# Kernel tuning notes

Measured on AMD Instinct MI355X. Metric: run time of the kernel, lower is better.

Reference implementation:

```python
import jax, jax.numpy as jnp
import numpy as np

C, H, K, G = 256, 8, 32, 8
HD = C // H
SCALE = HD ** -0.5
POS_BND = int(0.8 * K * 1 ** 0.5)  # 25
RPE_NUM = 2 * POS_BND + 1          # 51
NW = 4096


def setup_inputs() -> dict:
    key = jax.random.key(0)
    ks = jax.random.split(key, 8)
    data = jax.random.normal(ks[0], (NW * (K + G), C), dtype=jnp.float32)
    # relative xyz offsets between points in a window; exercise the clamp
    rel_pos = jax.random.randint(ks[1], (NW, K, K, 3), -POS_BND - 5, POS_BND + 6).astype(jnp.int32)
    # additive mask: 0 for valid pairs, -100 for masked (padded) pairs
    keep = jax.random.bernoulli(ks[2], 0.9, (NW, K + G, K + G))
    mask = jnp.where(keep, 0.0, -100.0).astype(jnp.float32)
    qkv_w = jax.random.normal(ks[3], (C, 3 * C), dtype=jnp.float32) * (C ** -0.5)
    qkv_b = jnp.zeros((3 * C,), dtype=jnp.float32)
    proj_w = jax.random.normal(ks[4], (C, C), dtype=jnp.float32) * (C ** -0.5)
    proj_b = jnp.zeros((C,), dtype=jnp.float32)
    rpe_table = jax.random.normal(ks[5], (3 * RPE_NUM, H), dtype=jnp.float32) * 0.02
    return {"data": data, "rel_pos": rel_pos, "mask": mask, "qkv_w": qkv_w,
            "qkv_b": qkv_b, "proj_w": proj_w, "proj_b": proj_b, "rpe_table": rpe_table}


def reference(data, rel_pos, mask, qkv_w, qkv_b, proj_w, proj_b, rpe_table):
    W = K + G  # window size including context tokens
    qkv = data @ qkv_w + qkv_b                              # (T, 3C)
    qkv_std = jnp.std(qkv, axis=0, ddof=1)                  # torch .std is unbiased
    qkv = qkv.reshape(-1, W, 3, H, HD).transpose(2, 0, 3, 1, 4)  # (3, Nw, H, W, HD)
    q, k, v = qkv[0] * SCALE, qkv[1], qkv[2]
    attn = jnp.einsum('nhqd,nhkd->nhqk', q, k)              # (Nw, H, W, W)
    # RPE: clamp offsets, index per-axis slices of table, sum over xyz
    idx = jnp.clip(rel_pos, -POS_BND, POS_BND) + POS_BND + jnp.arange(3, dtype=rel_pos.dtype) * RPE_NUM
    rpe = rpe_table[idx].sum(axis=3)                        # (Nw, K, K, H)
    rpe = rpe.transpose(0, 3, 1, 2)                         # (Nw, H, K, K)
    rpe = jnp.pad(rpe, ((0, 0), (0, 0), (G, 0), (G, 0)))    # pad for context tokens
    attn = attn + rpe + mask[:, None]
    attn = jax.nn.softmax(attn, axis=-1)
    out = jnp.einsum('nhqk,nhkd->nqhd', attn, v).reshape(-1, W, C)
    out = out @ proj_w + proj_b                             # (Nw, W, C)
    return (out, qkv_std)
```

## Files before the change

kernel.cpp:

```cpp
#include <hip/hip_runtime.h>
#include <math.h>

#define SCALE_F 0.17677669529663687f

typedef __bf16 bf16x8 __attribute__((ext_vector_type(8)));
typedef float f32x4 __attribute__((ext_vector_type(4)));

__device__ __forceinline__ unsigned short f2bf(float f) {
  unsigned u = __builtin_bit_cast(unsigned, f);
  u = (u + 0x7FFFu + ((u >> 16) & 1u)) >> 16;
  return (unsigned short)u;
}
__device__ __forceinline__ float bf2f(unsigned short u) {
  return __builtin_bit_cast(float, (unsigned)u << 16);
}
__device__ __forceinline__ unsigned pk2(float a, float b) {
  return (unsigned)f2bf(a) | ((unsigned)f2bf(b) << 16);
}
__device__ __forceinline__ bf16x8 ld16(const void* p) {
  int4 v = *(const int4*)p;
  return __builtin_bit_cast(bf16x8, v);
}
__device__ __forceinline__ void gll16(const void* g, void* l) {
  __builtin_amdgcn_global_load_lds(
      (const __attribute__((address_space(1))) unsigned int*)g,
      (__attribute__((address_space(3))) unsigned int*)l, 16, 0, 0);
}


__global__ void octa_prep2(const float* __restrict__ qkv_w, const float* __restrict__ proj_w,
                           unsigned short* __restrict__ wTq, unsigned short* __restrict__ pTq)
{
  int e = blockIdx.x * 256 + threadIdx.x;
  if (e < 196608) {
    int c = e >> 13;
    int nc = c >> 3, kc = c & 7;
    int p2 = e & 8191;
    int n = p2 >> 5, cw = p2 & 31;
    int kl = cw ^ (((n >> 1) & 3) << 3);
    wTq[e] = f2bf(qkv_w[(size_t)(kc * 32 + kl) * 768 + nc * 256 + n]);
  } else {
    int e2 = e - 196608;
    int kc = e2 >> 13, p2 = e2 & 8191;
    int n = p2 >> 5, cw = p2 & 31;
    int kl = cw ^ (((n >> 1) & 3) << 3);
    pTq[e2] = f2bf(proj_w[(size_t)(kc * 32 + kl) * 256 + n]);
  }
}

#define KQ_A0 0
#define KQ_A1 8192
#define KQ_B0 16384
#define KQ_B1 32768
#define KQ_LDS 49152

__global__ __launch_bounds__(512, 4)
void octa_qkv(const float* __restrict__ data, const float* __restrict__ qkv_b,
              const unsigned short* __restrict__ wTq, float* __restrict__ ws,
              char* __restrict__ qg, char* __restrict__ kg, char* __restrict__ vg)
{
  extern __shared__ char smem[];
  const int tid = threadIdx.x, lane = tid & 63, wid = tid >> 6;
  const int ql = lane & 15, lg = lane >> 4;
  const int bm = blockIdx.x / 3, nc = blockIdx.x - bm * 3;
  const int wr = wid >> 2, wc = wid & 3;
  const char* wbase = (const char*)wTq + (size_t)nc * 131072;

  const int arow = tid >> 2, aq = tid & 3;
  const float* abase = data + ((size_t)bm * 128 + arow) * 256 + aq * 8;
  const int alds = arow * 64 + ((aq * 16) ^ (((arow >> 1) & 3) << 4));

  float4 a0 = *(const float4*)abase;
  float4 a1 = *(const float4*)(abase + 4);
  gll16(wbase + wid * 1024 + lane * 16, smem + KQ_B0 + wid * 1024);
  gll16(wbase + 8192 + wid * 1024 + lane * 16, smem + KQ_B0 + 8192 + wid * 1024);
  *(uint2*)(smem + KQ_A0 + alds) = make_uint2(pk2(a0.x, a0.y), pk2(a0.z, a0.w));
  *(uint2*)(smem + KQ_A0 + alds + 8) = make_uint2(pk2(a1.x, a1.y), pk2(a1.z, a1.w));
  __syncthreads();

  f32x4 acc[4][4];
  #pragma unroll
  for (int m = 0; m < 4; ++m)
    #pragma unroll
    for (int n = 0; n < 4; ++n) acc[m][n] = (f32x4){0.f, 0.f, 0.f, 0.f};

  #pragma unroll
  for (int t = 0; t < 8; ++t) {
    float4 na0, na1;
    if (t < 7) {
      na0 = *(const float4*)(abase + (t + 1) * 32);
      na1 = *(const float4*)(abase + (t + 1) * 32 + 4);
      const char* bsrc = wbase + (size_t)(t + 1) * 16384;
      char* bb1 = smem + (((t + 1) & 1) ? KQ_B1 : KQ_B0);
      gll16(bsrc + wid * 1024 + lane * 16, bb1 + wid * 1024);
      gll16(bsrc + 8192 + wid * 1024 + lane * 16, bb1 + 8192 + wid * 1024);
    }
    const char* ab = smem + ((t & 1) ? KQ_A1 : KQ_A0);
    const char* bb = smem + ((t & 1) ? KQ_B1 : KQ_B0);
    bf16x8 af[4], bf[4];
    #pragma unroll
    for (int mt = 0; mt < 4; ++mt) {
      int row = wr * 64 + mt * 16 + ql;
      af[mt] = ld16(ab + row * 64 + ((lg * 16) ^ (((row >> 1) & 3) << 4)));
    }
    #pragma unroll
    for (int nt = 0; nt < 4; ++nt) {
      int n = wc * 64 + nt * 16 + ql;
      bf[nt] = ld16(bb + n * 64 + ((lg * 16) ^ (((n >> 1) & 3) << 4)));
    }
    #pragma unroll
    for (int nt = 0; nt < 4; ++nt)
      #pragma unroll
      for (int mt = 0; mt < 4; ++mt)
        acc[mt][nt] = __builtin_amdgcn_mfma_f32_16x16x32_bf16(af[mt], bf[nt], acc[mt][nt], 0, 0, 0);
    if (t < 7) {
      char* ab1 = smem + (((t + 1) & 1) ? KQ_A1 : KQ_A0);
      *(uint2*)(ab1 + alds) = make_uint2(pk2(na0.x, na0.y), pk2(na0.z, na0.w));
      *(uint2*)(ab1 + alds + 8) = make_uint2(pk2(na1.x, na1.y), pk2(na1.z, na1.w));
    }
    __syncthreads();
  }

  char* base = nc == 0 ? qg : (nc == 1 ? kg : vg);
  const float cs = (nc == 0) ? SCALE_F : 1.0f;
  #pragma unroll
  for (int nt = 0; nt < 4; ++nt) {
    int col = wc * 64 + nt * 16 + ql;
    int h = col >> 5, d = col & 31;
    float bias = qkv_b[nc * 256 + col];
    float s1 = 0.f, s2 = 0.f;
    #pragma unroll
    for (int mt = 0; mt < 4; ++mt) {
      int tg0 = bm * 128 + wr * 64 + mt * 16 + lg * 4;
      int w = tg0 / 40, tk0 = tg0 - w * 40;
      size_t slice = (size_t)(w * 8 + h) * 2560;
      #pragma unroll
      for (int r = 0; r < 4; ++r) {
        float v = acc[mt][nt][r] + bias;
        s1 += v; s2 += v * v;
        *(unsigned short*)(base + slice + (tk0 + r) * 64 + d * 2) = f2bf(v * cs);
      }
    }
    s1 += __shfl_xor(s1, 16); s1 += __shfl_xor(s1, 32);
    s2 += __shfl_xor(s2, 16); s2 += __shfl_xor(s2, 32);
    if (lg == 0) {
      atomicAdd(ws + nc * 256 + col, s1);
      atomicAdd(ws + 768 + nc * 256 + col, s2);
    }
  }
}

#define A2_MSK 0
#define A2_IDX 4160
#define A2_RPT 8256
#define A2_P   13376
#define A2_LDS 44096

__global__ __launch_bounds__(512, 4)
void octa_attn(const char* __restrict__ qg, const char* __restrict__ kg,
               const char* __restrict__ vg, const float* __restrict__ maskp,
               const int* __restrict__ rel_pos, const float* __restrict__ rpe_table,
               char* __restrict__ Og)
{
  extern __shared__ char smem[];
  const int tid = threadIdx.x, w = blockIdx.x, wid = tid >> 6;
  const int lane = tid & 63, ql = lane & 15, lg = lane >> 4, h = wid;
  const int perm = ql * 64 + lg * 16;
  const char* qb = qg + (size_t)(w * 8 + h) * 2560;
  const char* kb = kg + (size_t)(w * 8 + h) * 2560;
  const char* vb = vg + (size_t)(w * 8 + h) * 2560;

  bf16x8 kf0 = ld16(kb + perm), kf1 = ld16(kb + 1024 + perm), kf2 = ld16(kb + 2048 + perm);
  bf16x8 qf0 = ld16(qb + perm), qf1 = ld16(qb + 1024 + perm), qf2 = ld16(qb + 2048 + perm);
  union U8 { unsigned short u[8]; bf16x8 v; };
  U8 ua, ub, uc, ud;
  #pragma unroll
  for (int j = 0; j < 8; ++j) {
    int tok = lg * 8 + j;
    ua.u[j] = *(const unsigned short*)(vb + tok * 64 + ql * 2);
    ub.u[j] = *(const unsigned short*)(vb + tok * 64 + (16 + ql) * 2);
  }
  if (lg == 0) {
    #pragma unroll
    for (int j = 0; j < 8; ++j) {
      uc.u[j] = *(const unsigned short*)(vb + (32 + j) * 64 + ql * 2);
      ud.u[j] = *(const unsigned short*)(vb + (32 + j) * 64 + (16 + ql) * 2);
    }
  } else {
    #pragma unroll
    for (int j = 0; j < 8; ++j) { uc.u[j] = 0; ud.u[j] = 0; }
  }
  bf16x8 vA = ua.v, vB = ub.v, vC = uc.v, vD = ud.v;

  for (int f = tid; f < 1600; f += 512) {
    float m = maskp[(size_t)w * 1600 + f];
    int qi = f / 40, kj = f - qi * 40;
    *(unsigned short*)(smem + A2_MSK + kj * 104 + qi * 2) = f2bf(m);
  }
  for (int f = tid; f < 1024; f += 512) {
    const int* rp = rel_pos + ((size_t)w * 1024 + f) * 3;
    int c0 = rp[0], c1 = rp[1], c2 = rp[2];
    c0 = min(25, max(-25, c0)); c1 = min(25, max(-25, c1)); c2 = min(25, max(-25, c2));
    unsigned pk = (unsigned)(c0 + 25) | ((unsigned)(c1 + 76) << 10) | ((unsigned)(c2 + 127) << 20);
    int qi8 = f >> 5, kj8 = f & 31;
    *(unsigned*)(smem + A2_IDX + kj8 * 128 + ((qi8 * 4) ^ ((kj8 & 1) << 6))) = pk;
  }
  for (int f = tid; f < 1224; f += 512)
    *(float*)(smem + A2_RPT + (((f & 7) * 160 + (f >> 3)) << 2)) = rpe_table[f];
  __syncthreads();

  f32x4 st[9];
  {
    bf16x8 kf[3] = {kf0, kf1, kf2}, qf[3] = {qf0, qf1, qf2};
    #pragma unroll
    for (int a = 0; a < 3; ++a)
      #pragma unroll
      for (int b = 0; b < 3; ++b)
        st[a * 3 + b] = __builtin_amdgcn_mfma_f32_16x16x32_bf16(
            kf[a], qf[b], (f32x4){0.f, 0.f, 0.f, 0.f}, 0, 0, 0);
  }

  float mx[3] = {-3e38f, -3e38f, -3e38f};
  #pragma unroll
  for (int a = 0; a < 3; ++a) {
    #pragma unroll
    for (int b = 0; b < 3; ++b) {
      #pragma unroll
      for (int r = 0; r < 4; ++r) {
        int kj = a * 16 + lg * 4 + r;
        int qi = b * 16 + ql;
        float s = st[a * 3 + b][r];
        if (kj < 40) {
          if (qi < 40) {
            s += bf2f(*(const unsigned short*)(smem + A2_MSK + kj * 104 + qi * 2));
            if (kj >= 8 && qi >= 8) {
              unsigned pk = *(const unsigned*)(smem + A2_IDX + (kj - 8) * 128 +
                                               (((qi - 8) * 4) ^ (((kj - 8) & 1) << 6)));
              s += *(const float*)(smem + A2_RPT + ((h * 160 + (pk & 1023)) << 2))
                 + *(const float*)(smem + A2_RPT + ((h * 160 + ((pk >> 10) & 1023)) << 2))
                 + *(const float*)(smem + A2_RPT + ((h * 160 + (pk >> 20)) << 2));
            }
          }
        } else {
          s = -1e30f;
        }
        st[a * 3 + b][r] = s;
        mx[b] = fmaxf(mx[b], s);
      }
    }
  }
  #pragma unroll
  for (int b = 0; b < 3; ++b) {
    mx[b] = fmaxf(mx[b], __shfl_xor(mx[b], 16));
    mx[b] = fmaxf(mx[b], __shfl_xor(mx[b], 32));
  }
  float sum[3] = {0.f, 0.f, 0.f};
  #pragma unroll
  for (int a = 0; a < 3; ++a)
    #pragma unroll
    for (int b = 0; b < 3; ++b)
      #pragma unroll
      for (int r = 0; r < 4; ++r) {
        float e = __expf(st[a * 3 + b][r] - mx[b]);
        st[a * 3 + b][r] = e;
        sum[b] += e;
      }
  float inv[3];
  #pragma unroll
  for (int b = 0; b < 3; ++b) {
    sum[b] += __shfl_xor(sum[b], 16);
    sum[b] += __shfl_xor(sum[b], 32);
    inv[b] = 1.f / sum[b];
  }

  char* pb_ = smem + A2_P + wid * 3840;
  f32x4 ot[6];
  #pragma unroll
  for (int i = 0; i < 6; ++i) ot[i] = (f32x4){0.f, 0.f, 0.f, 0.f};

  #pragma unroll
  for (int a = 0; a < 2; ++a)
    #pragma unroll
    for (int b = 0; b < 3; ++b)
      #pragma unroll
      for (int r = 0; r < 4; ++r) {
        int kj = a * 16 + lg * 4 + r, qi = b * 16 + ql;
        *(unsigned short*)(pb_ + qi * 80 + kj * 2) = f2bf(st[a * 3 + b][r] * inv[b]);
      }
  asm volatile("" ::: "memory");
  #pragma unroll
  for (int b = 0; b < 3; ++b) {
    bf16x8 pf = ld16(pb_ + (b * 16 + ql) * 80 + lg * 16);
    ot[b]     = __builtin_amdgcn_mfma_f32_16x16x32_bf16(vA, pf, ot[b], 0, 0, 0);
    ot[3 + b] = __builtin_amdgcn_mfma_f32_16x16x32_bf16(vB, pf, ot[3 + b], 0, 0, 0);
  }
  asm volatile("" ::: "memory");
  #pragma unroll
  for (int b = 0; b < 3; ++b) {
    int qi = b * 16 + ql;
    #pragma unroll
    for (int r = 0; r < 4; ++r)
      *(unsigned short*)(pb_ + qi * 80 + (lg * 4 + r) * 2) = f2bf(st[6 + b][r] * inv[b]);
    *(uint2*)(pb_ + qi * 80 + 32 + lg * 8) = make_uint2(0u, 0u);
  }
  asm volatile("" ::: "memory");
  #pragma unroll
  for (int b = 0; b < 3; ++b) {
    bf16x8 pf = ld16(pb_ + (b * 16 + ql) * 80 + lg * 16);
    ot[b]     = __builtin_amdgcn_mfma_f32_16x16x32_bf16(vC, pf, ot[b], 0, 0, 0);
    ot[3 + b] = __builtin_amdgcn_mfma_f32_16x16x32_bf16(vD, pf, ot[3 + b], 0, 0, 0);
  }

  __syncthreads();
  #pragma unroll
  for (int dm = 0; dm < 2; ++dm)
    #pragma unroll
    for (int b = 0; b < 3; ++b) {
      int qi = b * 16 + ql;
      if (b == 2 && ql >= 8) continue;
      unsigned u0 = pk2(ot[dm * 3 + b][0], ot[dm * 3 + b][1]);
      unsigned u1 = pk2(ot[dm * 3 + b][2], ot[dm * 3 + b][3]);
      int tg = w * 40 + qi;
      int colb = (h * 32 + dm * 16 + lg * 4) * 2;
      *(uint2*)(Og + (size_t)tg * 512 + (colb ^ (((tg >> 1) & 3) << 4))) = make_uint2(u0, u1);
    }
}

#define P3_A0 0
#define P3_A1 8192
#define P3_B0 16384
#define P3_B1 32768
#define P3_LDS 49152

__global__ __launch_bounds__(512, 4)
void octa_proj(const char* __restrict__ Og, const unsigned short* __restrict__ pTq,
               const float* __restrict__ proj_b, float* __restrict__ out)
{
  extern __shared__ char smem[];
  const int tid = threadIdx.x, lane = tid & 63, wid = tid >> 6;
  const int ql = lane & 15, lg = lane >> 4;
  const int bm = blockIdx.x;
  const int wr = wid >> 2, wc = wid & 3;
  const char* pbase = (const char*)pTq;

  gll16(Og + ((size_t)bm * 128 + (tid >> 2)) * 512 + (tid & 3) * 16,
        smem + P3_A0 + wid * 1024);
  #pragma unroll
  for (int it = 0; it < 2; ++it)
    gll16(pbase + (wid * 128 + it * 64 + lane) * 16, smem + P3_B0 + wid * 2048 + it * 1024);
  __syncthreads();

  f32x4 acc[4][4];
  #pragma unroll
  for (int m = 0; m < 4; ++m)
    #pragma unroll
    for (int n = 0; n < 4; ++n) acc[m][n] = (f32x4){0.f, 0.f, 0.f, 0.f};

  #pragma unroll
  for (int t = 0; t < 8; ++t) {
    if (t < 7) {
      char* ab1 = smem + (((t + 1) & 1) ? P3_A1 : P3_A0);
      char* bb1 = smem + (((t + 1) & 1) ? P3_B1 : P3_B0);
      gll16(Og + ((size_t)bm * 128 + (tid >> 2)) * 512 + (t + 1) * 64 + (tid & 3) * 16,
            ab1 + wid * 1024);
      #pragma unroll
      for (int it = 0; it < 2; ++it)
        gll16(pbase + (size_t)(t + 1) * 16384 + (wid * 128 + it * 64 + lane) * 16,
              bb1 + wid * 2048 + it * 1024);
    }
    const char* ab = smem + ((t & 1) ? P3_A1 : P3_A0);
    const char* bb = smem + ((t & 1) ? P3_B1 : P3_B0);
    bf16x8 af[4];
    #pragma unroll
    for (int mt = 0; mt < 4; ++mt) {
      int row = wr * 64 + mt * 16 + ql;
      af[mt] = ld16(ab + row * 64 + ((lg * 16) ^ (((row >> 1) & 3) << 4)));
    }
    #pragma unroll
    for (int nt = 0; nt < 4; ++nt) {
      int n = wc * 64 + nt * 16 + ql;
      bf16x8 bf = ld16(bb + n * 64 + ((lg * 16) ^ (((n >> 1) & 3) << 4)));
      #pragma unroll
      for (int mt = 0; mt < 4; ++mt)
        acc[mt][nt] = __builtin_amdgcn_mfma_f32_16x16x32_bf16(af[mt], bf, acc[mt][nt], 0, 0, 0);
    }
    __syncthreads();
  }

  #pragma unroll
  for (int nt = 0; nt < 4; ++nt) {
    int col = wc * 64 + nt * 16 + ql;
    float pb = proj_b[col];
    #pragma unroll
    for (int mt = 0; mt < 4; ++mt)
      #pragma unroll
      for (int r = 0; r < 4; ++r) {
        int tg = bm * 128 + wr * 64 + mt * 16 + lg * 4 + r;
        out[(size_t)tg * 256 + col] = acc[mt][nt][r] + pb;
      }
  }
}

__global__ void octa_std(const float* __restrict__ ws, float* __restrict__ out,
                         int total_rows, size_t off)
{
  int j = blockIdx.x * 256 + threadIdx.x;
  if (j < 768) {
    float s = ws[j], ss = ws[768 + j];
    float T = (float)total_rows;
    float var = (ss - s * s / T) / (T - 1.f);
    out[off + j] = sqrtf(fmaxf(var, 0.f));
  }
}

#define O_RPE 0
#define O_MSK 4896
#define O_IDX 8096
#define O_A   12192
#define O_ATT 36768
#define B1_SZ 49152
#define ATT_STRIDE 11776
#define AK 3840
#define AV 7680
#define B2_S (O_ATT + 94208)
#define B2_A O_ATT
#define LDS_BYTES_V4 163744

__device__ __forceinline__ int a_addr(int row, int byte) {
  return O_A + row * 512 + (byte ^ ((row & 7) << 4));
}
__device__ __forceinline__ int v_addr(int d, int byte) {
  return AV + d * 128 + (byte ^ ((d & 7) << 4));
}

__global__ void octa_prep_v4(const float* __restrict__ qkv_w, const float* __restrict__ proj_w,
                             unsigned short* __restrict__ wTq, unsigned short* __restrict__ pTq)
{
  int idx = blockIdx.x * 256 + threadIdx.x;
  if (idx < 196608) {
    int n = idx >> 8, k = idx & 255;
    wTq[idx] = f2bf(qkv_w[k * 768 + n]);
  } else {
    int i = idx - 196608;
    int n = i >> 8, k = i & 255;
    pTq[i] = f2bf(proj_w[k * 256 + n]);
  }
}

__global__ __launch_bounds__(512, 2)
void octa_main_v4(const float* __restrict__ data, const int* __restrict__ rel_pos,
                  const float* __restrict__ maskp, const float* __restrict__ qkv_b,
                  const float* __restrict__ proj_b, const float* __restrict__ rpe_table,
                  const unsigned short* __restrict__ wTq, const unsigned short* __restrict__ pTq,
                  float* __restrict__ ws, float* __restrict__ out)
{
  extern __shared__ char smem[];
  float* s_rpe = (float*)(smem + O_RPE);
  const int tid = threadIdx.x;
  const int w   = blockIdx.x;
  const int wid = tid >> 6;
  const int lane = tid & 63;
  const int ql = lane & 15;
  const int lg = lane >> 4;
  const int h  = wid;
  const int ab = O_ATT + wid * ATT_STRIDE;

  {
    #pragma unroll
    for (int it = 0; it < 6; ++it) {
      int g = it * 512 + tid;
      int n = g >> 2, slot = g & 3;
      const char* src = (const char*)wTq + (size_t)n * 512 + ((slot * 16) ^ ((n & 3) << 4));
      gll16(src, smem + O_ATT + it * 8192 + wid * 1024);
    }
  }
  for (int f = tid; f < 1224; f += 512) s_rpe[f] = rpe_table[f];
  for (int f = tid; f < 400; f += 512) {
    float4 m4 = ((const float4*)(maskp + (size_t)w * 1600))[f];
    uint2 pk;
    pk.x = pk2(m4.x, m4.y); pk.y = pk2(m4.z, m4.w);
    *(uint2*)(smem + O_MSK + f * 8) = pk;
  }
  for (int p = tid; p < 1024; p += 512) {
    const int* rp = rel_pos + ((size_t)w * 1024 + p) * 3;
    int c0 = rp[0], c1 = rp[1], c2 = rp[2];
    c0 = min(25, max(-25, c0)); c1 = min(25, max(-25, c1)); c2 = min(25, max(-25, c2));
    unsigned pk = (unsigned)(c0 + 25) | ((unsigned)(c1 + 76) << 10) | ((unsigned)(c2 + 127) << 20);
    *(unsigned*)(smem + O_IDX + ((p * 4) ^ (((p >> 5) & 7) << 4))) = pk;
  }
  {
    const float4* src = (const float4*)(data + (size_t)w * 10240);
    for (int f = tid; f < 2560; f += 512) {
      int token = f >> 6, q4 = f & 63;
      float4 d4 = src[f];
      uint2 pk;
      pk.x = pk2(d4.x, d4.y); pk.y = pk2(d4.z, d4.w);
      *(uint2*)(smem + a_addr(token, q4 * 8)) = pk;
    }
    int token = 40 + (tid >> 6), byte = (tid & 63) * 8;
    *(uint2*)(smem + a_addr(token, byte)) = make_uint2(0u, 0u);
  }
  __syncthreads();

  f32x4 acc[18];
  #pragma unroll
  for (int i = 0; i < 18; ++i) acc[i] = (f32x4){0.f, 0.f, 0.f, 0.f};

  for (int t = 0; t < 8; ++t) {
    if (t < 7) {
      int bb = O_ATT + ((t + 1) & 1) * B1_SZ;
      #pragma unroll
      for (int it = 0; it < 6; ++it) {
        int g = it * 512 + tid;
        int n = g >> 2, slot = g & 3;
        const char* src = (const char*)wTq + (size_t)n * 512 + (t + 1) * 64
                          + ((slot * 16) ^ ((n & 3) << 4));
        gll16(src, smem + bb + it * 8192 + wid * 1024);
      }
    }
    const int bb = O_ATT + (t & 1) * B1_SZ;
    bf16x8 af[3];
    #pragma unroll
    for (int mt = 0; mt < 3; ++mt)
      af[mt] = ld16(smem + a_addr(mt * 16 + ql, t * 64 + lg * 16));
    #pragma unroll
    for (int j = 0; j < 6; ++j) {
      int n = ((j >> 1) * 16 + 2 * wid + (j & 1)) * 16 + ql;
      bf16x8 bf = ld16(smem + bb + n * 64 + ((lg * 16) ^ ((n & 3) << 4)));
      #pragma unroll
      for (int mt = 0; mt < 3; ++mt)
        acc[j * 3 + mt] = __builtin_amdgcn_mfma_f32_16x16x32_bf16(af[mt], bf, acc[j * 3 + mt], 0, 0, 0);
    }
    __syncthreads();
  }

  {
    #pragma unroll
    for (int it = 0; it < 4; ++it) {
      int g = it * 512 + tid;
      int n = g >> 3, slot = g & 7;
      const char* src = (const char*)pTq + (size_t)n * 512 + ((slot * 16) ^ ((n & 7) << 4));
      gll16(src, smem + B2_S + it * 8192 + wid * 1024);
    }
  }

  #pragma unroll
  for (int j = 0; j < 6; ++j) {
    int sec = j >> 1;
    int ncol = sec * 256 + 32 * wid + (j & 1) * 16 + ql;
    int d = (j & 1) * 16 + ql;
    float bias = qkv_b[ncol];
// ... 66 lines not shown
        mx[b] = fmaxf(mx[b], s);
      }
    }
  }
  #pragma unroll
  for (int b = 0; b < 3; ++b) {
    mx[b] = fmaxf(mx[b], __shfl_xor(mx[b], 16));
    mx[b] = fmaxf(mx[b], __shfl_xor(mx[b], 32));
  }
  float sum[3] = {0.f, 0.f, 0.f};
  #pragma unroll
  for (int a = 0; a < 3; ++a)
    #pragma unroll
    for (int b = 0; b < 3; ++b)
      #pragma unroll
      for (int r = 0; r < 4; ++r) {
        float e = __expf(st[a * 3 + b][r] - mx[b]);
        st[a * 3 + b][r] = e;
        sum[b] += e;
      }
  float inv[3];
  #pragma unroll
  for (int b = 0; b < 3; ++b) {
    sum[b] += __shfl_xor(sum[b], 16);
    sum[b] += __shfl_xor(sum[b], 32);
    inv[b] = 1.f / sum[b];
  }

  f32x4 ot[6];
  #pragma unroll
  for (int i = 0; i < 6; ++i) ot[i] = (f32x4){0.f, 0.f, 0.f, 0.f};

  #pragma unroll
  for (int a = 0; a < 2; ++a)
    #pragma unroll
    for (int b = 0; b < 3; ++b)
      #pragma unroll
      for (int r = 0; r < 4; ++r) {
        int kj = a * 16 + lg * 4 + r, qi = b * 16 + ql;
        *(unsigned short*)(smem + ab + qi * 80 + kj * 2) = f2bf(st[a * 3 + b][r] * inv[b]);
      }
  asm volatile("" ::: "memory");
  {
    bf16x8 vf0 = ld16(smem + ab + v_addr(ql, lg * 16));
    bf16x8 vf1 = ld16(smem + ab + v_addr(16 + ql, lg * 16));
    #pragma unroll
    for (int b = 0; b < 3; ++b) {
      bf16x8 pf = ld16(smem + ab + (b * 16 + ql) * 80 + lg * 16);
      ot[b] = __builtin_amdgcn_mfma_f32_16x16x32_bf16(vf0, pf, ot[b], 0, 0, 0);
      ot[3 + b] = __builtin_amdgcn_mfma_f32_16x16x32_bf16(vf1, pf, ot[3 + b], 0, 0, 0);
    }
  }
  asm volatile("" ::: "memory");
  #pragma unroll
  for (int b = 0; b < 3; ++b) {
    int qi = b * 16 + ql;
    #pragma unroll
    for (int r = 0; r < 4; ++r) {
      int kj = 32 + lg * 4 + r;
      *(unsigned short*)(smem + ab + qi * 80 + (kj - 32) * 2) = f2bf(st[6 + b][r] * inv[b]);
    }
    *(uint2*)(smem + ab + qi * 80 + 32 + lg * 8) = make_uint2(0u, 0u);
  }
  asm volatile("" ::: "memory");
  {
    bf16x8 vf0 = ld16(smem + ab + v_addr(ql, 64 + lg * 16));
    bf16x8 vf1 = ld16(smem + ab + v_addr(16 + ql, 64 + lg * 16));
    #pragma unroll
    for (int b = 0; b < 3; ++b) {
      bf16x8 pf = ld16(smem + ab + (b * 16 + ql) * 80 + lg * 16);
      ot[b] = __builtin_amdgcn_mfma_f32_16x16x32_bf16(vf0, pf, ot[b], 0, 0, 0);
      ot[3 + b] = __builtin_amdgcn_mfma_f32_16x16x32_bf16(vf1, pf, ot[3 + b], 0, 0, 0);
    }
  }
  #pragma unroll
  for (int dm = 0; dm < 2; ++dm)
    #pragma unroll
    for (int b = 0; b < 3; ++b)
      #pragma unroll
      for (int r = 0; r < 4; ++r) {
        int d = dm * 16 + lg * 4 + r;
        int qi = b * 16 + ql;
        *(unsigned short*)(smem + a_addr(qi, (h * 32 + d) * 2)) = f2bf(ot[dm * 3 + b][r]);
      }
  __syncthreads();

  f32x4 oacc[6];
  #pragma unroll
  for (int i = 0; i < 6; ++i) oacc[i] = (f32x4){0.f, 0.f, 0.f, 0.f};

  for (int t = 0; t < 4; ++t) {
    if (t < 3) {
      int bb = ((t + 1) & 1) ? B2_A : B2_S;
      #pragma unroll
      for (int it = 0; it < 4; ++it) {
        int g = it * 512 + tid;
        int n = g >> 3, slot = g & 7;
        const char* src = (const char*)pTq + (size_t)n * 512 + (t + 1) * 128
                          + ((slot * 16) ^ ((n & 7) << 4));
        gll16(src, smem + bb + it * 8192 + wid * 1024);
      }
    }
    const int bb = (t & 1) ? B2_A : B2_S;
    #pragma unroll
    for (int ks = 0; ks < 2; ++ks) {
      bf16x8 af[3];
      #pragma unroll
      for (int mt = 0; mt < 3; ++mt)
        af[mt] = ld16(smem + a_addr(mt * 16 + ql, t * 128 + ks * 64 + lg * 16));
      #pragma unroll
      for (int nt = 0; nt < 2; ++nt) {
        int n = (2 * wid + nt) * 16 + ql;
        bf16x8 bf = ld16(smem + bb + n * 128 + ((ks * 64 + lg * 16) ^ ((n & 7) << 4)));
        #pragma unroll
        for (int mt = 0; mt < 3; ++mt)
          oacc[nt * 3 + mt] = __builtin_amdgcn_mfma_f32_16x16x32_bf16(af[mt], bf, oacc[nt * 3 + mt], 0, 0, 0);
      }
    }
    __syncthreads();
  }

  #pragma unroll
  for (int nt = 0; nt < 2; ++nt) {
    int ncol = (2 * wid + nt) * 16 + ql;
    float pb = proj_b[ncol];
    #pragma unroll
    for (int mt = 0; mt < 3; ++mt)
      #pragma unroll
      for (int r = 0; r < 4; ++r) {
        int token = mt * 16 + lg * 4 + r;
        if (token < 40)
          out[(size_t)w * 10240 + token * 256 + ncol] = oacc[nt * 3 + mt][r] + pb;
      }
  }
}

extern "C" void kernel_launch(void* const* d_in, const int* in_sizes, int n_in,
                              void* d_out, int out_size, void* d_ws, size_t ws_size,
                              hipStream_t stream) {
  const float* data    = (const float*)d_in[0];
  const int*   rel_pos = (const int*)d_in[1];
  const float* maskp   = (const float*)d_in[2];
  const float* qkv_w   = (const float*)d_in[3];
  const float* qkv_b   = (const float*)d_in[4];
  const float* proj_w  = (const float*)d_in[5];
  const float* proj_b  = (const float*)d_in[6];
  const float* rpe_tab = (const float*)d_in[7];
  float* out = (float*)d_out;
  float* ws  = (float*)d_ws;

  const int nw = in_sizes[1] / 3072;
  const int total_rows = nw * 40;
  const size_t std_off = (size_t)nw * 10240;

  const size_t WS_NEED = 530432ull + 83886080ull;

  unsigned short* wTq = (unsigned short*)((char*)d_ws + 6144);
  unsigned short* pTq = (unsigned short*)((char*)d_ws + 399360);

  hipMemsetAsync(ws, 0, 6144, stream);

  if (ws_size >= WS_NEED) {
    char* kg = (char*)d_ws + 530432;
    char* Og = kg;
    char* qg = (char*)d_out;
    char* vg = (char*)d_out + 83886080;

    hipLaunchKernelGGL(octa_prep2, dim3(1024), dim3(256), 0, stream, qkv_w, proj_w, wTq, pTq);
    hipLaunchKernelGGL(octa_qkv, dim3(nw * 40 / 128 * 3), dim3(512), KQ_LDS, stream,
                       data, qkv_b, wTq, ws, qg, kg, vg);
    hipLaunchKernelGGL(octa_attn, dim3(nw), dim3(512), A2_LDS, stream,
                       qg, kg, vg, maskp, rel_pos, rpe_tab, Og);
    hipLaunchKernelGGL(octa_proj, dim3(nw * 40 / 128), dim3(512), P3_LDS, stream,
                       Og, pTq, proj_b, out);
    hipLaunchKernelGGL(octa_std, dim3(3), dim3(256), 0, stream, ws, out, total_rows, std_off);
  } else {
    hipLaunchKernelGGL(octa_prep_v4, dim3(1024), dim3(256), 0, stream, qkv_w, proj_w, wTq, pTq);
    (void)hipFuncSetAttribute((const void*)octa_main_v4,
                              hipFuncAttributeMaxDynamicSharedMemorySize, LDS_BYTES_V4);
    hipLaunchKernelGGL(octa_main_v4, dim3(nw), dim3(512), LDS_BYTES_V4, stream,
                       data, rel_pos, maskp, qkv_b, proj_b, rpe_tab, wTq, pTq, ws, out);
    hipLaunchKernelGGL(octa_std, dim3(3), dim3(256), 0, stream, ws, out, total_rows, std_off);
  }
}
```

Baseline: 381.2 us.

## Fuse attention and output projection into one kernel per window

Adds a kernel that runs windowed attention and then, in the same block, multiplies the bf16 attention output held in LDS by the projection weights, which are double-buffered through global_load_lds. This removes the round trip of the attention output through global memory and one kernel launch. Q, K and V now go to separate workspace buffers instead of aliasing the output buffer, so the fused path needs a larger workspace and falls back to the old path when it is not available. It also adds s_setprio around the MFMA blocks in both attention kernels. The fused kernel uses more LDS (57 KB) and runs an 8-step loop with barriers, which may lower occupancy.

```diff
diff --git a/kernel.cpp b/kernel.cpp
--- a/kernel.cpp
+++ b/kernel.cpp
@@ -150,6 +150,247 @@
   }
 }
 
+#define F_MSK 0
+#define F_IDX 4160
+#define F_RPT 8256
+#define F_P   13376
+#define F_O   0
+#define F_B0  24576
+#define F_B1  40960
+#define F_LDS 57344
+
+__global__ __launch_bounds__(512, 4)
+void octa_attnproj(const char* __restrict__ qg, const char* __restrict__ kg,
+                   const char* __restrict__ vg, const float* __restrict__ maskp,
+                   const int* __restrict__ rel_pos, const float* __restrict__ rpe_table,
+                   const unsigned short* __restrict__ pTq, const float* __restrict__ proj_b,
+                   float* __restrict__ out)
+{
+  extern __shared__ char smem[];
+  const int tid = threadIdx.x, w = blockIdx.x, wid = tid >> 6;
+  const int lane = tid & 63, ql = lane & 15, lg = lane >> 4, h = wid;
+  const int perm = ql * 64 + lg * 16;
+  const char* qb = qg + (size_t)(w * 8 + h) * 2560;
+  const char* kb = kg + (size_t)(w * 8 + h) * 2560;
+  const char* vb = vg + (size_t)(w * 8 + h) * 2560;
+
+  bf16x8 kf0 = ld16(kb + perm), kf1 = ld16(kb + 1024 + perm), kf2 = ld16(kb + 2048 + perm);
+  bf16x8 qf0 = ld16(qb + perm), qf1 = ld16(qb + 1024 + perm), qf2 = ld16(qb + 2048 + perm);
+  union U8 { unsigned short u[8]; bf16x8 v; };
+  U8 ua, ub, uc, ud;
+  #pragma unroll
+  for (int j = 0; j < 8; ++j) {
+    int tok = lg * 8 + j;
+    ua.u[j] = *(const unsigned short*)(vb + tok * 64 + ql * 2);
+    ub.u[j] = *(const unsigned short*)(vb + tok * 64 + (16 + ql) * 2);
+  }
+  if (lg == 0) {
+    #pragma unroll
+    for (int j = 0; j < 8; ++j) {
+      uc.u[j] = *(const unsigned short*)(vb + (32 + j) * 64 + ql * 2);
+      ud.u[j] = *(const unsigned short*)(vb + (32 + j) * 64 + (16 + ql) * 2);
+    }
+  } else {
+    #pragma unroll
+    for (int j = 0; j < 8; ++j) { uc.u[j] = 0; ud.u[j] = 0; }
+  }
+  bf16x8 vA = ua.v, vB = ub.v, vC = uc.v, vD = ud.v;
+
+  for (int f = tid; f < 1600; f += 512) {
+    float m = maskp[(size_t)w * 1600 + f];
+    int qi = f / 40, kj = f - qi * 40;
+    *(unsigned short*)(smem + F_MSK + kj * 104 + qi * 2) = f2bf(m);
+  }
+  for (int f = tid; f < 1024; f += 512) {
+    const int* rp = rel_pos + ((size_t)w * 1024 + f) * 3;
+    int c0 = rp[0], c1 = rp[1], c2 = rp[2];
+    c0 = min(25, max(-25, c0)); c1 = min(25, max(-25, c1)); c2 = min(25, max(-25, c2));
+    unsigned pk = (unsigned)(c0 + 25) | ((unsigned)(c1 + 76) << 10) | ((unsigned)(c2 + 127) << 20);
+    int qi8 = f >> 5, kj8 = f & 31;
+    *(unsigned*)(smem + F_IDX + kj8 * 128 + ((qi8 * 4) ^ ((kj8 & 1) << 6))) = pk;
+  }
+  for (int f = tid; f < 1224; f += 512)
+    *(float*)(smem + F_RPT + (((f & 7) * 160 + (f >> 3)) << 2)) = rpe_table[f];
+  __syncthreads();
+
+  f32x4 st[9];
+  {
+    bf16x8 kf[3] = {kf0, kf1, kf2}, qf[3] = {qf0, qf1, qf2};
+    __builtin_amdgcn_s_setprio(1);
+    #pragma unroll
+    for (int a = 0; a < 3; ++a)
+      #pragma unroll
+      for (int b = 0; b < 3; ++b)
+        st[a * 3 + b] = __builtin_amdgcn_mfma_f32_16x16x32_bf16(
+            kf[a], qf[b], (f32x4){0.f, 0.f, 0.f, 0.f}, 0, 0, 0);
+    __builtin_amdgcn_s_setprio(0);
+  }
+
+  float mx[3] = {-3e38f, -3e38f, -3e38f};
+  #pragma unroll
+  for (int a = 0; a < 3; ++a) {
+    #pragma unroll
+    for (int b = 0; b < 3; ++b) {
+      #pragma unroll
+      for (int r = 0; r < 4; ++r) {
+        int kj = a * 16 + lg * 4 + r;
+        int qi = b * 16 + ql;
+        float s = st[a * 3 + b][r];
+        if (kj < 40) {
+          if (qi < 40) {
+            s += bf2f(*(const unsigned short*)(smem + F_MSK + kj * 104 + qi * 2));
+            if (kj >= 8 && qi >= 8) {
+              unsigned pk = *(const unsigned*)(smem + F_IDX + (kj - 8) * 128 +
+                                               (((qi - 8) * 4) ^ (((kj - 8) & 1) << 6)));
+              s += *(const float*)(smem + F_RPT + ((h * 160 + (pk & 1023)) << 2))
+                 + *(const float*)(smem + F_RPT + ((h * 160 + ((pk >> 10) & 1023)) << 2))
+                 + *(const float*)(smem + F_RPT + ((h * 160 + (pk >> 20)) << 2));
+            }
+          }
+        } else {
+          s = -1e30f;
+        }
+        st[a * 3 + b][r] = s;
+        mx[b] = fmaxf(mx[b], s);
+      }
+    }
+  }
+  #pragma unroll
+  for (int b = 0; b < 3; ++b) {
+    mx[b] = fmaxf(mx[b], __shfl_xor(mx[b], 16));
+    mx[b] = fmaxf(mx[b], __shfl_xor(mx[b], 32));
+  }
+  float sum[3] = {0.f, 0.f, 0.f};
+  #pragma unroll
+  for (int a = 0; a < 3; ++a)
+    #pragma unroll
+    for (int b = 0; b < 3; ++b)
+      #pragma unroll
+      for (int r = 0; r < 4; ++r) {
+        float e = __expf(st[a * 3 + b][r] - mx[b]);
+        st[a * 3 + b][r] = e;
+        sum[b] += e;
+      }
+  float inv[3];
+  #pragma unroll
+  for (int b = 0; b < 3; ++b) {
+    sum[b] += __shfl_xor(sum[b], 16);
+    sum[b] += __shfl_xor(sum[b], 32);
+    inv[b] = 1.f / sum[b];
+  }
+
+  char* pb_ = smem + F_P + wid * 3840;
+  f32x4 ot[6];
+  #pragma unroll
+  for (int i = 0; i < 6; ++i) ot[i] = (f32x4){0.f, 0.f, 0.f, 0.f};
+
+  #pragma unroll
+  for (int a = 0; a < 2; ++a)
+    #pragma unroll
+    for (int b = 0; b < 3; ++b)
+      #pragma unroll
+      for (int r = 0; r < 4; ++r) {
+        int kj = a * 16 + lg * 4 + r, qi = b * 16 + ql;
+        *(unsigned short*)(pb_ + qi * 80 + kj * 2) = f2bf(st[a * 3 + b][r] * inv[b]);
+      }
+  asm volatile("" ::: "memory");
+  __builtin_amdgcn_s_setprio(1);
+  #pragma unroll
+  for (int b = 0; b < 3; ++b) {
+    bf16x8 pf = ld16(pb_ + (b * 16 + ql) * 80 + lg * 16);
+    ot[b]     = __builtin_amdgcn_mfma_f32_16x16x32_bf16(vA, pf, ot[b], 0, 0, 0);
+    ot[3 + b] = __builtin_amdgcn_mfma_f32_16x16x32_bf16(vB, pf, ot[3 + b], 0, 0, 0);
+  }
+  __builtin_amdgcn_s_setprio(0);
+  asm volatile("" ::: "memory");
+  #pragma unroll
+  for (int b = 0; b < 3; ++b) {
+    int qi = b * 16 + ql;
+    #pragma unroll
+    for (int r = 0; r < 4; ++r)
+      *(unsigned short*)(pb_ + qi * 80 + (lg * 4 + r) * 2) = f2bf(st[6 + b][r] * inv[b]);
+    *(uint2*)(pb_ + qi * 80 + 32 + lg * 8) = make_uint2(0u, 0u);
+  }
+  asm volatile("" ::: "memory");
+  __builtin_amdgcn_s_setprio(1);
+  #pragma unroll
+  for (int b = 0; b < 3; ++b) {
+    bf16x8 pf = ld16(pb_ + (b * 16 + ql) * 80 + lg * 16);
+    ot[b]     = __builtin_amdgcn_mfma_f32_16x16x32_bf16(vC, pf, ot[b], 0, 0, 0);
+    ot[3 + b] = __builtin_amdgcn_mfma_f32_16x16x32_bf16(vD, pf, ot[3 + b], 0, 0, 0);
+  }
+  __builtin_amdgcn_s_setprio(0);
+
+  __syncthreads();
+  #pragma unroll
+  for (int it = 0; it < 2; ++it)
+    gll16((const char*)pTq + (wid * 128 + it * 64 + lane) * 16,
+          smem + F_B0 + wid * 2048 + it * 1024);
+  #pragma unroll
+  for (int dm = 0; dm < 2; ++dm)
+    #pragma unroll
+    for (int b = 0; b < 3; ++b) {
+      int qi = b * 16 + ql;
+      unsigned u0 = pk2(ot[dm * 3 + b][0], ot[dm * 3 + b][1]);
+      unsigned u1 = pk2(ot[dm * 3 + b][2], ot[dm * 3 + b][3]);
+      int colb = (h * 32 + dm * 16 + lg * 4) * 2;
+      *(uint2*)(smem + F_O + qi * 512 + (colb ^ ((qi & 7) << 4))) = make_uint2(u0, u1);
+    }
+  __syncthreads();
+
+  f32x4 pacc[3][2];
+  #pragma unroll
+  for (int m = 0; m < 3; ++m)
+    #pragma unroll
+    for (int n = 0; n < 2; ++n) pacc[m][n] = (f32x4){0.f, 0.f, 0.f, 0.f};
+  const int c0 = wid * 32;
+
+  #pragma unroll
+  for (int t = 0; t < 8; ++t) {
+    if (t < 7) {
+      char* bb1 = smem + (((t + 1) & 1) ? F_B1 : F_B0);
+      #pragma unroll
+      for (int it = 0; it < 2; ++it)
+        gll16((const char*)pTq + (size_t)(t + 1) * 16384 + (wid * 128 + it * 64 + lane) * 16,
+              bb1 + wid * 2048 + it * 1024);
+    }
+    const char* bb = smem + ((t & 1) ? F_B1 : F_B0);
+    bf16x8 af[3], bfr[2];
+    #pragma unroll
+    for (int mt = 0; mt < 3; ++mt) {
+      int row = mt * 16 + ql;
+      af[mt] = ld16(smem + F_O + row * 512 + ((t * 64 + lg * 16) ^ ((row & 7) << 4)));
+    }
+    #pragma unroll
+    for (int nt = 0; nt < 2; ++nt) {
+      int n = c0 + nt * 16 + ql;
+      bfr[nt] = ld16(bb + n * 64 + ((lg * 16) ^ (((n >> 1) & 3) << 4)));
+    }
+    __builtin_amdgcn_s_setprio(1);
+    #pragma unroll
+    for (int nt = 0; nt < 2; ++nt)
+      #pragma unroll
+      for (int mt = 0; mt < 3; ++mt)
+        pacc[mt][nt] = __builtin_amdgcn_mfma_f32_16x16x32_bf16(af[mt], bfr[nt], pacc[mt][nt], 0, 0, 0);
+    __builtin_amdgcn_s_setprio(0);
+    __syncthreads();
+  }
+
+  #pragma unroll
+  for (int nt = 0; nt < 2; ++nt) {
+    int col = c0 + nt * 16 + ql;
+    float pb = proj_b[col];
+    #pragma unroll
+    for (int mt = 0; mt < 3; ++mt)
+      #pragma unroll
+      for (int r = 0; r < 4; ++r) {
+        int row = mt * 16 + lg * 4 + r;
+        if (row < 40)
+          out[(size_t)(w * 40 + row) * 256 + col] = pacc[mt][nt][r] + pb;
+      }
+  }
+}
+
 #define A2_MSK 0
 #define A2_IDX 4160
 #define A2_RPT 8256
@@ -212,12 +453,14 @@
   f32x4 st[9];
   {
     bf16x8 kf[3] = {kf0, kf1, kf2}, qf[3] = {qf0, qf1, qf2};
+    __builtin_amdgcn_s_setprio(1);
     #pragma unroll
     for (int a = 0; a < 3; ++a)
       #pragma unroll
       for (int b = 0; b < 3; ++b)
         st[a * 3 + b] = __builtin_amdgcn_mfma_f32_16x16x32_bf16(
             kf[a], qf[b], (f32x4){0.f, 0.f, 0.f, 0.f}, 0, 0, 0);
+    __builtin_amdgcn_s_setprio(0);
   }
 
   float mx[3] = {-3e38f, -3e38f, -3e38f};
@@ -288,12 +531,14 @@
         *(unsigned short*)(pb_ + qi * 80 + kj * 2) = f2bf(st[a * 3 + b][r] * inv[b]);
       }
   asm volatile("" ::: "memory");
+  __builtin_amdgcn_s_setprio(1);
   #pragma unroll
   for (int b = 0; b < 3; ++b) {
     bf16x8 pf = ld16(pb_ + (b * 16 + ql) * 80 + lg * 16);
     ot[b]     = __builtin_amdgcn_mfma_f32_16x16x32_bf16(vA, pf, ot[b], 0, 0, 0);
     ot[3 + b] = __builtin_amdgcn_mfma_f32_16x16x32_bf16(vB, pf, ot[3 + b], 0, 0, 0);
   }
+  __builtin_amdgcn_s_setprio(0);
   asm volatile("" ::: "memory");
   #pragma unroll
   for (int b = 0; b < 3; ++b) {
@@ -304,12 +549,14 @@
     *(uint2*)(pb_ + qi * 80 + 32 + lg * 8) = make_uint2(0u, 0u);
   }
   asm volatile("" ::: "memory");
+  __builtin_amdgcn_s_setprio(1);
   #pragma unroll
   for (int b = 0; b < 3; ++b) {
     bf16x8 pf = ld16(pb_ + (b * 16 + ql) * 80 + lg * 16);
     ot[b]     = __builtin_amdgcn_mfma_f32_16x16x32_bf16(vC, pf, ot[b], 0, 0, 0);
     ot[3 + b] = __builtin_amdgcn_mfma_f32_16x16x32_bf16(vD, pf, ot[3 + b], 0, 0, 0);
   }
+  __builtin_amdgcn_s_setprio(0);
 
   __syncthreads();
   #pragma unroll
@@ -769,19 +1016,33 @@
   const int nw = in_sizes[1] / 3072;
   const int total_rows = nw * 40;
   const size_t std_off = (size_t)nw * 10240;
-
-  const size_t WS_NEED = 530432ull + 83886080ull;
+  const size_t SZ = 83886080ull;
+
+  const size_t WS1 = 530432ull + 3ull * SZ + 4096ull;
+  const size_t WS2 = 530432ull + SZ;
 
   unsigned short* wTq = (unsigned short*)((char*)d_ws + 6144);
   unsigned short* pTq = (unsigned short*)((char*)d_ws + 399360);
 
   hipMemsetAsync(ws, 0, 6144, stream);
 
-  if (ws_size >= WS_NEED) {
+  if (ws_size >= WS1) {
+    char* qg = (char*)d_ws + 530432;
+    char* kg = qg + SZ;
+    char* vg = kg + SZ;
+    (void)hipFuncSetAttribute((const void*)octa_attnproj,
+                              hipFuncAttributeMaxDynamicSharedMemorySize, F_LDS);
+    hipLaunchKernelGGL(octa_prep2, dim3(1024), dim3(256), 0, stream, qkv_w, proj_w, wTq, pTq);
+    hipLaunchKernelGGL(octa_qkv, dim3(nw * 40 / 128 * 3), dim3(512), KQ_LDS, stream,
+                       data, qkv_b, wTq, ws, qg, kg, vg);
+    hipLaunchKernelGGL(octa_attnproj, dim3(nw), dim3(512), F_LDS, stream,
+                       qg, kg, vg, maskp, rel_pos, rpe_tab, pTq, proj_b, out);
+    hipLaunchKernelGGL(octa_std, dim3(3), dim3(256), 0, stream, ws, out, total_rows, std_off);
+  } else if (ws_size >= WS2) {
     char* kg = (char*)d_ws + 530432;
     char* Og = kg;
     char* qg = (char*)d_out;
-    char* vg = (char*)d_out + 83886080;
+    char* vg = (char*)d_out + SZ;
 
     hipLaunchKernelGGL(octa_prep2, dim3(1024), dim3(256), 0, stream, qkv_w, proj_w, wTq, pTq);
     hipLaunchKernelGGL(octa_qkv, dim3(nw * 40 / 128 * 3), dim3(512), KQ_LDS, stream,
```

Result: faster. 365.5 us (-4.1%).

## Fuse attention with output projection and precompute per-window bias in separate kernel

Applied to the files above, without the earlier changes.

Adds a kernel that combines mask and gathered RPE into a bf16 per-head bias tensor stored in the output buffer. The attention kernel then reads this bias instead of building LDS tables, and performs the output projection in-block, reading proj weights directly from global memory. This removes the intermediate attention-output round trip and the separate projection launch, and adds s_setprio around MFMA sections. In exchange it adds bias tensor traffic, a larger workspace requirement for q/k/v, and an unstaged B-operand load path.

```diff
diff --git a/kernel.cpp b/kernel.cpp
--- a/kernel.cpp
+++ b/kernel.cpp
@@ -48,6 +48,42 @@
   }
 }
 
+__global__ __launch_bounds__(256)
+void octa_bias(const float* __restrict__ maskp, const int* __restrict__ rel_pos,
+               const float* __restrict__ rpe_table, char* __restrict__ biasg)
+{
+  __shared__ char bl[25600];
+  const int w = blockIdx.x, tid = threadIdx.x;
+  for (int e = tid; e < 1600; e += 256) {
+    int qi = e / 40, kj = e - qi * 40;
+    float m = maskp[(size_t)w * 1600 + qi * 40 + kj];
+    float b8[8];
+    if (qi >= 8 && kj >= 8) {
+      const int* rp = rel_pos + ((size_t)w * 1024 + (qi - 8) * 32 + (kj - 8)) * 3;
+      int c0 = rp[0], c1 = rp[1], c2 = rp[2];
+      c0 = min(25, max(-25, c0)); c1 = min(25, max(-25, c1)); c2 = min(25, max(-25, c2));
+      const float4* r0 = (const float4*)(rpe_table + (c0 + 25) * 8);
+      const float4* r1 = (const float4*)(rpe_table + (c1 + 76) * 8);
+      const float4* r2 = (const float4*)(rpe_table + (c2 + 127) * 8);
+      float4 a0 = r0[0], a1 = r1[0], a2 = r2[0];
+      float4 b0 = r0[1], b1 = r1[1], b2 = r2[1];
+      b8[0] = m + a0.x + a1.x + a2.x; b8[1] = m + a0.y + a1.y + a2.y;
+      b8[2] = m + a0.z + a1.z + a2.z; b8[3] = m + a0.w + a1.w + a2.w;
+      b8[4] = m + b0.x + b1.x + b2.x; b8[5] = m + b0.y + b1.y + b2.y;
+      b8[6] = m + b0.z + b1.z + b2.z; b8[7] = m + b0.w + b1.w + b2.w;
+    } else {
+      #pragma unroll
+      for (int h = 0; h < 8; ++h) b8[h] = m;
+    }
+    #pragma unroll
+    for (int h = 0; h < 8; ++h)
+      *(unsigned short*)(bl + h * 3200 + kj * 80 + qi * 2) = f2bf(b8[h]);
+  }
+  __syncthreads();
+  for (int f = tid; f < 1600; f += 256)
+    *(int4*)(biasg + (size_t)w * 40960 + f * 16) = *(const int4*)(bl + f * 16);
+}
+
 #define KQ_A0 0
 #define KQ_A1 8192
 #define KQ_B0 16384
@@ -150,17 +186,13 @@
   }
 }
 
-#define A2_MSK 0
-#define A2_IDX 4160
-#define A2_RPT 8256
-#define A2_P   13376
-#define A2_LDS 44096
+#define F2_LDS 30720
 
 __global__ __launch_bounds__(512, 4)
-void octa_attn(const char* __restrict__ qg, const char* __restrict__ kg,
-               const char* __restrict__ vg, const float* __restrict__ maskp,
-               const int* __restrict__ rel_pos, const float* __restrict__ rpe_table,
-               char* __restrict__ Og)
+void octa_attnproj2(const char* __restrict__ qg, const char* __restrict__ kg,
+                    const char* __restrict__ vg, const char* __restrict__ biasg,
+                    const unsigned short* __restrict__ pTq, const float* __restrict__ proj_b,
+                    float* __restrict__ out)
 {
   extern __shared__ char smem[];
   const int tid = threadIdx.x, w = blockIdx.x, wid = tid >> 6;
@@ -169,6 +201,7 @@
   const char* qb = qg + (size_t)(w * 8 + h) * 2560;
   const char* kb = kg + (size_t)(w * 8 + h) * 2560;
   const char* vb = vg + (size_t)(w * 8 + h) * 2560;
+  const char* bb_ = biasg + (size_t)w * 40960 + h * 3200;
 
   bf16x8 kf0 = ld16(kb + perm), kf1 = ld16(kb + 1024 + perm), kf2 = ld16(kb + 2048 + perm);
   bf16x8 qf0 = ld16(qb + perm), qf1 = ld16(qb + 1024 + perm), qf2 = ld16(qb + 2048 + perm);
@@ -192,32 +225,17 @@
   }
   bf16x8 vA = ua.v, vB = ub.v, vC = uc.v, vD = ud.v;
 
-  for (int f = tid; f < 1600; f += 512) {
-    float m = maskp[(size_t)w * 1600 + f];
-    int qi = f / 40, kj = f - qi * 40;
-    *(unsigned short*)(smem + A2_MSK + kj * 104 + qi * 2) = f2bf(m);
-  }
-  for (int f = tid; f < 1024; f += 512) {
-    const int* rp = rel_pos + ((size_t)w * 1024 + f) * 3;
-    int c0 = rp[0], c1 = rp[1], c2 = rp[2];
-    c0 = min(25, max(-25, c0)); c1 = min(25, max(-25, c1)); c2 = min(25, max(-25, c2));
-    unsigned pk = (unsigned)(c0 + 25) | ((unsigned)(c1 + 76) << 10) | ((unsigned)(c2 + 127) << 20);
-    int qi8 = f >> 5, kj8 = f & 31;
-    *(unsigned*)(smem + A2_IDX + kj8 * 128 + ((qi8 * 4) ^ ((kj8 & 1) << 6))) = pk;
-  }
-  for (int f = tid; f < 1224; f += 512)
-    *(float*)(smem + A2_RPT + (((f & 7) * 160 + (f >> 3)) << 2)) = rpe_table[f];
-  __syncthreads();
-
   f32x4 st[9];
   {
     bf16x8 kf[3] = {kf0, kf1, kf2}, qf[3] = {qf0, qf1, qf2};
+    __builtin_amdgcn_s_setprio(1);
     #pragma unroll
     for (int a = 0; a < 3; ++a)
       #pragma unroll
       for (int b = 0; b < 3; ++b)
         st[a * 3 + b] = __builtin_amdgcn_mfma_f32_16x16x32_bf16(
             kf[a], qf[b], (f32x4){0.f, 0.f, 0.f, 0.f}, 0, 0, 0);
+    __builtin_amdgcn_s_setprio(0);
   }
 
   float mx[3] = {-3e38f, -3e38f, -3e38f};
@@ -231,16 +249,8 @@
         int qi = b * 16 + ql;
         float s = st[a * 3 + b][r];
         if (kj < 40) {
-          if (qi < 40) {
-            s += bf2f(*(const unsigned short*)(smem + A2_MSK + kj * 104 + qi * 2));
-            if (kj >= 8 && qi >= 8) {
-              unsigned pk = *(const unsigned*)(smem + A2_IDX + (kj - 8) * 128 +
-                                               (((qi - 8) * 4) ^ (((kj - 8) & 1) << 6)));
-              s += *(const float*)(smem + A2_RPT + ((h * 160 + (pk & 1023)) << 2))
-                 + *(const float*)(smem + A2_RPT + ((h * 160 + ((pk >> 10) & 1023)) << 2))
-                 + *(const float*)(smem + A2_RPT + ((h * 160 + (pk >> 20)) << 2));
-            }
-          }
+          if (qi < 40)
+            s += bf2f(*(const unsigned short*)(bb_ + kj * 80 + qi * 2));
         } else {
           s = -1e30f;
         }
@@ -273,7 +283,7 @@
     inv[b] = 1.f / sum[b];
   }
 
-  char* pb_ = smem + A2_P + wid * 3840;
+  char* pb_ = smem + wid * 3840;
   f32x4 ot[6];
   #pragma unroll
   for (int i = 0; i < 6; ++i) ot[i] = (f32x4){0.f, 0.f, 0.f, 0.f};
@@ -288,12 +298,14 @@
         *(unsigned short*)(pb_ + qi * 80 + kj * 2) = f2bf(st[a * 3 + b][r] * inv[b]);
       }
   asm volatile("" ::: "memory");
+  __builtin_amdgcn_s_setprio(1);
   #pragma unroll
   for (int b = 0; b < 3; ++b) {
     bf16x8 pf = ld16(pb_ + (b * 16 + ql) * 80 + lg * 16);
     ot[b]     = __builtin_amdgcn_mfma_f32_16x16x32_bf16(vA, pf, ot[b], 0, 0, 0);
     ot[3 + b] = __builtin_amdgcn_mfma_f32_16x16x32_bf16(vB, pf, ot[3 + b], 0, 0, 0);
   }
+  __builtin_amdgcn_s_setprio(0);
   asm volatile("" ::: "memory");
   #pragma unroll
   for (int b = 0; b < 3; ++b) {
@@ -304,12 +316,14 @@
     *(uint2*)(pb_ + qi * 80 + 32 + lg * 8) = make_uint2(0u, 0u);
   }
   asm volatile("" ::: "memory");
+  __builtin_amdgcn_s_setprio(1);
   #pragma unroll
   for (int b = 0; b < 3; ++b) {
     bf16x8 pf = ld16(pb_ + (b * 16 + ql) * 80 + lg * 16);
     ot[b]     = __builtin_amdgcn_mfma_f32_16x16x32_bf16(vC, pf, ot[b], 0, 0, 0);
     ot[3 + b] = __builtin_amdgcn_mfma_f32_16x16x32_bf16(vD, pf, ot[3 + b], 0, 0, 0);
   }
+  __builtin_amdgcn_s_setprio(0);
 
   __syncthreads();
   #pragma unroll
@@ -317,86 +331,54 @@
     #pragma unroll
     for (int b = 0; b < 3; ++b) {
       int qi = b * 16 + ql;
-      if (b == 2 && ql >= 8) continue;
       unsigned u0 = pk2(ot[dm * 3 + b][0], ot[dm * 3 + b][1]);
       unsigned u1 = pk2(ot[dm * 3 + b][2], ot[dm * 3 + b][3]);
-      int tg = w * 40 + qi;
       int colb = (h * 32 + dm * 16 + lg * 4) * 2;
-      *(uint2*)(Og + (size_t)tg * 512 + (colb ^ (((tg >> 1) & 3) << 4))) = make_uint2(u0, u1);
-    }
-}
-
-#define P3_A0 0
-#define P3_A1 8192
-#define P3_B0 16384
-#define P3_B1 32768
-#define P3_LDS 49152
-
-__global__ __launch_bounds__(512, 4)
-void octa_proj(const char* __restrict__ Og, const unsigned short* __restrict__ pTq,
-               const float* __restrict__ proj_b, float* __restrict__ out)
-{
-  extern __shared__ char smem[];
-  const int tid = threadIdx.x, lane = tid & 63, wid = tid >> 6;
-  const int ql = lane & 15, lg = lane >> 4;
-  const int bm = blockIdx.x;
-  const int wr = wid >> 2, wc = wid & 3;
-  const char* pbase = (const char*)pTq;
-
-  gll16(Og + ((size_t)bm * 128 + (tid >> 2)) * 512 + (tid & 3) * 16,
-        smem + P3_A0 + wid * 1024);
-  #pragma unroll
-  for (int it = 0; it < 2; ++it)
-    gll16(pbase + (wid * 128 + it * 64 + lane) * 16, smem + P3_B0 + wid * 2048 + it * 1024);
+      *(uint2*)(smem + qi * 512 + (colb ^ ((qi & 7) << 4))) = make_uint2(u0, u1);
+    }
   __syncthreads();
 
-  f32x4 acc[4][4];
-  #pragma unroll
-  for (int m = 0; m < 4; ++m)
-    #pragma unroll
-    for (int n = 0; n < 4; ++n) acc[m][n] = (f32x4){0.f, 0.f, 0.f, 0.f};
+  f32x4 pacc[3][2];
+  #pragma unroll
+  for (int m = 0; m < 3; ++m)
+    #pragma unroll
+    for (int n = 0; n < 2; ++n) pacc[m][n] = (f32x4){0.f, 0.f, 0.f, 0.f};
+  const int c0 = wid * 32;
+  const char* pB = (const char*)pTq;
 
   #pragma unroll
   for (int t = 0; t < 8; ++t) {
-    if (t < 7) {
-      char* ab1 = smem + (((t + 1) & 1) ? P3_A1 : P3_A0);
-      char* bb1 = smem + (((t + 1) & 1) ? P3_B1 : P3_B0);
-      gll16(Og + ((size_t)bm * 128 + (tid >> 2)) * 512 + (t + 1) * 64 + (tid & 3) * 16,
-            ab1 + wid * 1024);
-      #pragma unroll
-      for (int it = 0; it < 2; ++it)
-        gll16(pbase + (size_t)(t + 1) * 16384 + (wid * 128 + it * 64 + lane) * 16,
-              bb1 + wid * 2048 + it * 1024);
-    }
-    const char* ab = smem + ((t & 1) ? P3_A1 : P3_A0);
-    const char* bb = smem + ((t & 1) ? P3_B1 : P3_B0);
-    bf16x8 af[4];
-    #pragma unroll
-    for (int mt = 0; mt < 4; ++mt) {
-      int row = wr * 64 + mt * 16 + ql;
-      af[mt] = ld16(ab + row * 64 + ((lg * 16) ^ (((row >> 1) & 3) << 4)));
-    }
-    #pragma unroll
-    for (int nt = 0; nt < 4; ++nt) {
-      int n = wc * 64 + nt * 16 + ql;
-      bf16x8 bf = ld16(bb + n * 64 + ((lg * 16) ^ (((n >> 1) & 3) << 4)));
-      #pragma unroll
-      for (int mt = 0; mt < 4; ++mt)
-        acc[mt][nt] = __builtin_amdgcn_mfma_f32_16x16x32_bf16(af[mt], bf, acc[mt][nt], 0, 0, 0);
-    }
-    __syncthreads();
-  }
-
-  #pragma unroll
-  for (int nt = 0; nt < 4; ++nt) {
-    int col = wc * 64 + nt * 16 + ql;
+    bf16x8 af[3], bfr[2];
+    #pragma unroll
+    for (int mt = 0; mt < 3; ++mt) {
+      int row = mt * 16 + ql;
+      af[mt] = ld16(smem + row * 512 + ((t * 64 + lg * 16) ^ ((row & 7) << 4)));
+    }
+    #pragma unroll
+    for (int nt = 0; nt < 2; ++nt) {
+      int n = c0 + nt * 16 + ql;
+      bfr[nt] = ld16(pB + (size_t)t * 16384 + n * 64 + ((lg * 16) ^ (((n >> 1) & 3) << 4)));
+    }
+    __builtin_amdgcn_s_setprio(1);
+    #pragma unroll
+    for (int nt = 0; nt < 2; ++nt)
+      #pragma unroll
+      for (int mt = 0; mt < 3; ++mt)
+        pacc[mt][nt] = __builtin_amdgcn_mfma_f32_16x16x32_bf16(af[mt], bfr[nt], pacc[mt][nt], 0, 0, 0);
+    __builtin_amdgcn_s_setprio(0);
+  }
+
+  #pragma unroll
+  for (int nt = 0; nt < 2; ++nt) {
+    int col = c0 + nt * 16 + ql;
     float pb = proj_b[col];
     #pragma unroll
-    for (int mt = 0; mt < 4; ++mt)
-      #pragma unroll
-      for (int r = 0; r < 4; ++r) {
-        int tg = bm * 128 + wr * 64 + mt * 16 + lg * 4 + r;
-        out[(size_t)tg * 256 + col] = acc[mt][nt][r] + pb;
+    for (int mt = 0; mt < 3; ++mt)
+      #pragma unroll
+      for (int r = 0; r < 4; ++r) {
+        int row = mt * 16 + lg * 4 + r;
+        if (row < 40)
+          out[(size_t)(w * 40 + row) * 256 + col] = pacc[mt][nt][r] + pb;
       }
   }
 }
@@ -769,27 +751,29 @@
   const int nw = in_sizes[1] / 3072;
   const int total_rows = nw * 40;
   const size_t std_off = (size_t)nw * 10240;
-
-  const size_t WS_NEED = 530432ull + 83886080ull;
+  const size_t SZ = 83886080ull;
+
+  const size_t WS1 = 530432ull + 3ull * SZ + 4096ull;
 
   unsigned short* wTq = (unsigned short*)((char*)d_ws + 6144);
   unsigned short* pTq = (unsigned short*)((char*)d_ws + 399360);
 
   hipMemsetAsync(ws, 0, 6144, stream);
 
-  if (ws_size >= WS_NEED) {
-    char* kg = (char*)d_ws + 530432;
-    char* Og = kg;
-    char* qg = (char*)d_out;
-    char* vg = (char*)d_out + 83886080;
-
+  if (ws_size >= WS1) {
+    char* qg = (char*)d_ws + 530432;
+    char* kg = qg + SZ;
+    char* vg = kg + SZ;
+    char* biasg = (char*)d_out;
+    (void)hipFuncSetAttribute((const void*)octa_attnproj2,
+                              hipFuncAttributeMaxDynamicSharedMemorySize, F2_LDS);
     hipLaunchKernelGGL(octa_prep2, dim3(1024), dim3(256), 0, stream, qkv_w, proj_w, wTq, pTq);
+    hipLaunchKernelGGL(octa_bias, dim3(nw), dim3(256), 0, stream,
+                       maskp, rel_pos, rpe_tab, biasg);
     hipLaunchKernelGGL(octa_qkv, dim3(nw * 40 / 128 * 3), dim3(512), KQ_LDS, stream,
                        data, qkv_b, wTq, ws, qg, kg, vg);
-    hipLaunchKernelGGL(octa_attn, dim3(nw), dim3(512), A2_LDS, stream,
-                       qg, kg, vg, maskp, rel_pos, rpe_tab, Og);
-    hipLaunchKernelGGL(octa_proj, dim3(nw * 40 / 128), dim3(512), P3_LDS, stream,
-                       Og, pTq, proj_b, out);
+    hipLaunchKernelGGL(octa_attnproj2, dim3(nw), dim3(512), F2_LDS, stream,
+                       qg, kg, vg, biasg, pTq, proj_b, out);
     hipLaunchKernelGGL(octa_std, dim3(3), dim3(256), 0, stream, ws, out, total_rows, std_off);
   } else {
     hipLaunchKernelGGL(octa_prep_v4, dim3(1024), dim3(256), 0, stream, qkv_w, proj_w, wTq, pTq);
```

New measurement: 413.6 us. +8.5%, slower.
